# Kernel tuning notes

Measured on AMD Instinct MI355X. Metric: run time of the kernel, lower is better.

Reference implementation:

```python
import jax, jax.numpy as jnp
import numpy as np

N, CIN, H, W = 4, 64, 160, 256
INS_PER = 16
T = N * INS_PER            # total instances = sum(num_ins)
CH, OUT = 16, 1
WN = [(CIN + 2) * CH, CH * CH, CH * OUT]   # [1056, 256, 16]
BN = [CH, CH, OUT]
P = sum(WN) + sum(BN)      # 1361
MASK_BIAS_SHIFT = 2.19


def setup_inputs() -> dict:
    key = jax.random.key(0)
    k1, k2 = jax.random.split(key)
    x = jax.random.normal(k1, (N, CIN, H, W), dtype=jnp.float32)
    mask_head_params = jax.random.normal(k2, (T, P), dtype=jnp.float32) * 0.1
    num_ins = jnp.full((N,), INS_PER, dtype=jnp.int32)
    return {"x": x, "mask_head_params": mask_head_params, "num_ins": num_ins}


def reference(x, mask_head_params, num_ins):
    n, c, h, w = x.shape
    # compute_locations with stride=1: locations = stack((shift_x, shift_y)) + 0
    # NOTE: the original `locations[:0] /= H` / `locations[:1] /= W` are
    # zero-size slices (no-ops), so coords remain unnormalized.
    ys, xs = jnp.meshgrid(jnp.arange(h, dtype=jnp.float32),
                          jnp.arange(w, dtype=jnp.float32), indexing='ij')
    loc = jnp.stack([xs, ys], axis=0)                       # [2, H, W]
    loc = jnp.broadcast_to(loc[None], (n, 2, h, w))
    xc = jnp.concatenate([loc, x], axis=1)                  # [N, C+2, H, W]

    # per-image repeat -> one feature copy per instance
    feat = jnp.repeat(xc, num_ins, axis=0, total_repeat_length=T)  # [T, C+2, H, W]

    # parse dynamic params (mask=True: last bias shifted by -2.19)
    p = mask_head_params
    o = 0
    w0 = p[:, o:o + WN[0]].reshape(T, CH, CIN + 2); o += WN[0]
    w1 = p[:, o:o + WN[1]].reshape(T, CH, CH);      o += WN[1]
    w2 = p[:, o:o + WN[2]].reshape(T, OUT, CH);     o += WN[2]
    b0 = p[:, o:o + BN[0]]; o += BN[0]
    b1 = p[:, o:o + BN[1]]; o += BN[1]
    b2 = p[:, o:o + BN[2]] - MASK_BIAS_SHIFT

    # grouped 1x1 convs (groups=num_insts) == per-instance linear over HxW
    hdn = jax.nn.relu(jnp.einsum('toi,tihw->tohw', w0, feat) + b0[:, :, None, None])
    hdn = jax.nn.relu(jnp.einsum('toi,tihw->tohw', w1, hdn) + b1[:, :, None, None])
    out = jnp.einsum('toi,tihw->tohw', w2, hdn) + b2[:, :, None, None]
    return out.reshape(1, T * OUT, h, w)
```

## Files before the change

kernel.cpp:

```cpp
#include <hip/hip_runtime.h>


#define CIN  64
#define HH   160
#define WW   256
#define HWSZ (HH * WW)
#define PP   1361
#define MASK_BIAS_SHIFT 2.19f
#define PKF  2112
#define NSPLIT 2

typedef short short8 __attribute__((ext_vector_type(8)));
typedef float f32x4  __attribute__((ext_vector_type(4)));

union BF8 { short8 s; __bf16 b[8]; };


__global__ __launch_bounds__(64) void prep_params(
    const float* __restrict__ params, float* __restrict__ pk)
{
    const int t    = blockIdx.x;
    const int lane = threadIdx.x;
    const int col  = lane & 15;
    const int g    = lane >> 4;
    const float* pw = params + (size_t)t * PP;
    float* dst = pk + (size_t)t * PKF;

    BF8 a00, a01, a1;
#pragma unroll
    for (int j = 0; j < 8; ++j) {
        a00.b[j] = (__bf16)pw[col * 66 + 2 +      g * 8 + j];
        a01.b[j] = (__bf16)pw[col * 66 + 2 + 32 + g * 8 + j];
    }
#pragma unroll
    for (int j = 0; j < 4; ++j) {
        a1.b[j]     = (__bf16)pw[1056 + col * 16 + g * 4 + j];
        a1.b[4 + j] = (__bf16)0.f;
    }
    ((short8*)(dst      ))[lane] = a00.s;
    ((short8*)(dst + 256))[lane] = a01.s;
    ((short8*)(dst + 512))[lane] = a1.s;

    f32x4 wx, wy, b0, b1, w2;
#pragma unroll
    for (int j = 0; j < 4; ++j) {
        const int r = g * 4 + j;
        wx[j] = pw[r * 66 + 0];
        wy[j] = pw[r * 66 + 1];
        b0[j] = pw[1328 + r];
        b1[j] = pw[1344 + r];
        w2[j] = pw[1312 + r];
    }
    ((f32x4*)(dst +  768))[lane] = wx;
    ((f32x4*)(dst + 1024))[lane] = wy;
    ((f32x4*)(dst + 1280))[lane] = b0;
    ((f32x4*)(dst + 1536))[lane] = b1;
    ((f32x4*)(dst + 1792))[lane] = w2;
    if (lane == 0) dst[2048] = pw[1360] - MASK_BIAS_SHIFT;
}

__global__ __launch_bounds__(256, 4) void mask_head_mfma2(
    const float* __restrict__ x,
    const float* __restrict__ pk,
    const int*   __restrict__ num_ins,
    float*       __restrict__ out,
    int N, int T)
{
    const int tid  = threadIdx.x;
    const int wave = tid >> 6;
    const int lane = tid & 63;
    const int col  = lane & 15;
    const int g    = lane >> 4;
    const int n    = blockIdx.y;
    const int s    = blockIdx.z;
    const int pxw  = blockIdx.x * 256 + wave * 64;

    int t0 = 0;
    for (int j = 0; j < n; ++j) t0 += num_ins[j];
    int t1 = t0 + num_ins[n];
    if (n == N - 1) t1 = T;
    if (t1 > T) t1 = T;
    t0 = __builtin_amdgcn_readfirstlane(t0);
    t1 = __builtin_amdgcn_readfirstlane(t1);

    BF8 xb[4][2];
    const float* xbase = x + (size_t)n * CIN * HWSZ + pxw + col;
#pragma unroll
    for (int nt = 0; nt < 4; ++nt)
#pragma unroll
        for (int c = 0; c < 2; ++c)
#pragma unroll
            for (int j = 0; j < 8; ++j) {
                const int ch = c * 32 + g * 8 + j;
                xb[nt][c].b[j] = (__bf16)xbase[(size_t)ch * HWSZ + nt * 16];
            }

    float xf[4], yf[4];
#pragma unroll
    for (int nt = 0; nt < 4; ++nt) {
        const int pix = pxw + nt * 16 + col;
        xf[nt] = (float)(pix & (WW - 1));
        yf[nt] = (float)(pix >> 8);
    }

    for (int t = t0 + s; t < t1; t += NSPLIT) {
        const float* pt = pk + (size_t)t * PKF;

        short8 a00 = ((const short8*)(pt      ))[lane];
        short8 a01 = ((const short8*)(pt + 256))[lane];
        short8 a1  = ((const short8*)(pt + 512))[lane];
        f32x4  wxv = ((const f32x4*)(pt +  768))[lane];
        f32x4  wyv = ((const f32x4*)(pt + 1024))[lane];
        f32x4  b0v = ((const f32x4*)(pt + 1280))[lane];
        f32x4  b1v = ((const f32x4*)(pt + 1536))[lane];
        f32x4  w2v = ((const f32x4*)(pt + 1792))[lane];
        const float b2v = pt[2048];

        f32x4 acc0[4];
#pragma unroll
        for (int nt = 0; nt < 4; ++nt) {
            f32x4 a = {0.f, 0.f, 0.f, 0.f};
            a = __builtin_amdgcn_mfma_f32_16x16x32_bf16(a00, xb[nt][0].s, a, 0, 0, 0);
            a = __builtin_amdgcn_mfma_f32_16x16x32_bf16(a01, xb[nt][1].s, a, 0, 0, 0);
            acc0[nt] = a;
        }

        BF8 h0[4];
#pragma unroll
        for (int nt = 0; nt < 4; ++nt) {
#pragma unroll
            for (int j = 0; j < 4; ++j) {
                float v = acc0[nt][j] + b0v[j];
                v = fmaf(wxv[j], xf[nt], v);
                v = fmaf(wyv[j], yf[nt], v);
                v = fmaxf(v, 0.f);
                h0[nt].b[j]     = (__bf16)v;
                h0[nt].b[4 + j] = (__bf16)0.f;
            }
        }

        f32x4 acc1[4];
#pragma unroll
        for (int nt = 0; nt < 4; ++nt) {
            f32x4 a = {0.f, 0.f, 0.f, 0.f};
            acc1[nt] = __builtin_amdgcn_mfma_f32_16x16x32_bf16(a1, h0[nt].s, a, 0, 0, 0);
        }

        float oval = 0.f;
#pragma unroll
        for (int nt = 0; nt < 4; ++nt) {
            float sum = 0.f;
#pragma unroll
            for (int j = 0; j < 4; ++j) {
                const float h = fmaxf(acc1[nt][j] + b1v[j], 0.f);
                sum = fmaf(w2v[j], h, sum);
            }
            sum += __shfl_xor(sum, 16, 64);
            sum += __shfl_xor(sum, 32, 64);
            if (nt == g) oval = sum + b2v;
        }
        out[(size_t)t * HWSZ + pxw + lane] = oval;
    }
}

__global__ __launch_bounds__(256) void mask_head_mfma_nows(
    const float* __restrict__ x,
    const float* __restrict__ params,
    const int*   __restrict__ num_ins,
    float*       __restrict__ out,
    int N, int T)
{
    const int tid  = threadIdx.x;
    const int wave = tid >> 6;
    const int lane = tid & 63;
    const int col  = lane & 15;
    const int g    = lane >> 4;
    const int n    = blockIdx.y;
    const int pxw  = blockIdx.x * 256 + wave * 64;

    int t0 = 0;
    for (int j = 0; j < n; ++j) t0 += num_ins[j];
    int t1 = t0 + num_ins[n];
    if (n == N - 1) t1 = T;
    if (t1 > T) t1 = T;

    BF8 xb[4][2];
    const float* xbase = x + (size_t)n * CIN * HWSZ + pxw + col;
#pragma unroll
    for (int nt = 0; nt < 4; ++nt)
#pragma unroll
        for (int c = 0; c < 2; ++c)
#pragma unroll
            for (int j = 0; j < 8; ++j)
                xb[nt][c].b[j] = (__bf16)xbase[(size_t)(c * 32 + g * 8 + j) * HWSZ + nt * 16];

    float xf[4], yf[4];
#pragma unroll
    for (int nt = 0; nt < 4; ++nt) {
        const int pix = pxw + nt * 16 + col;
        xf[nt] = (float)(pix & (WW - 1));
        yf[nt] = (float)(pix >> 8);
    }

    for (int t = t0; t < t1; ++t) {
        const float* pw = params + (size_t)t * PP;
        BF8 a00, a01, a1;
#pragma unroll
        for (int j = 0; j < 8; ++j) {
            a00.b[j] = (__bf16)pw[col * 66 + 2 +      g * 8 + j];
            a01.b[j] = (__bf16)pw[col * 66 + 2 + 32 + g * 8 + j];
        }
#pragma unroll
        for (int j = 0; j < 4; ++j) {
            a1.b[j]     = (__bf16)pw[1056 + col * 16 + g * 4 + j];
            a1.b[4 + j] = (__bf16)0.f;
        }
        float wxv[4], wyv[4], b0v[4], b1v[4], w2v[4];
#pragma unroll
        for (int j = 0; j < 4; ++j) {
            const int r = g * 4 + j;
            wxv[j] = pw[r * 66 + 0];
            wyv[j] = pw[r * 66 + 1];
            b0v[j] = pw[1328 + r];
            b1v[j] = pw[1344 + r];
            w2v[j] = pw[1312 + r];
        }
        const float b2v = pw[1360] - MASK_BIAS_SHIFT;

        f32x4 acc0[4];
#pragma unroll
        for (int nt = 0; nt < 4; ++nt) {
            f32x4 a = {0.f, 0.f, 0.f, 0.f};
            a = __builtin_amdgcn_mfma_f32_16x16x32_bf16(a00.s, xb[nt][0].s, a, 0, 0, 0);
            a = __builtin_amdgcn_mfma_f32_16x16x32_bf16(a01.s, xb[nt][1].s, a, 0, 0, 0);
            acc0[nt] = a;
        }
        BF8 h0[4];
#pragma unroll
        for (int nt = 0; nt < 4; ++nt)
#pragma unroll
            for (int j = 0; j < 4; ++j) {
                float v = acc0[nt][j] + b0v[j];
                v = fmaf(wxv[j], xf[nt], v);
                v = fmaf(wyv[j], yf[nt], v);
                v = fmaxf(v, 0.f);
                h0[nt].b[j]     = (__bf16)v;
                h0[nt].b[4 + j] = (__bf16)0.f;
            }
        f32x4 acc1[4];
#pragma unroll
        for (int nt = 0; nt < 4; ++nt) {
            f32x4 a = {0.f, 0.f, 0.f, 0.f};
            acc1[nt] = __builtin_amdgcn_mfma_f32_16x16x32_bf16(a1.s, h0[nt].s, a, 0, 0, 0);
        }
        float oval = 0.f;
#pragma unroll
        for (int nt = 0; nt < 4; ++nt) {
            float sum = 0.f;
#pragma unroll
            for (int j = 0; j < 4; ++j) {
                const float h = fmaxf(acc1[nt][j] + b1v[j], 0.f);
                sum = fmaf(w2v[j], h, sum);
            }
            sum += __shfl_xor(sum, 16, 64);
            sum += __shfl_xor(sum, 32, 64);
            if (nt == g) oval = sum + b2v;
        }
        out[(size_t)t * HWSZ + pxw + lane] = oval;
    }
}

extern "C" void kernel_launch(void* const* d_in, const int* in_sizes, int n_in,
                              void* d_out, int out_size, void* d_ws, size_t ws_size,
                              hipStream_t stream) {
    const float* x      = (const float*)d_in[0];
    const float* params = (const float*)d_in[1];
    const int*   nins   = (const int*)d_in[2];
    float*       out    = (float*)d_out;

    const int N = in_sizes[2];
    const int T = in_sizes[1] / PP;
    const size_t ws_needed = (size_t)T * PKF * sizeof(float);

    if (ws_size >= ws_needed) {
        float* pk = (float*)d_ws;
        prep_params<<<T, dim3(64), 0, stream>>>(params, pk);
        dim3 grid(HWSZ / 256, N, NSPLIT);
        mask_head_mfma2<<<grid, dim3(256), 0, stream>>>(x, pk, nins, out, N, T);
    } else {
        dim3 grid(HWSZ / 256, N);
        mask_head_mfma_nows<<<grid, dim3(256), 0, stream>>>(x, params, nins, out, N, T);
    }
}
```

Measured before the change: 34.01 us.

## Stage block pixels in swizzled LDS and split instances across waves

Each block now converts its 256-pixel row of input features to bf16 once into XOR-swizzled shared memory. Each wave then handles a different subset of instances and covers all 256 pixels, instead of every wave covering its own 64 pixels for every instance. This aims to cut per-wave parameter loads and register pressure and to simplify the coordinate terms (y is constant per block). In exchange it adds 32KB of LDS per block, a block-wide barrier, and LDS reads inside the hot loop, and it may limit occupancy.

```diff
diff --git a/kernel.cpp b/kernel.cpp
--- a/kernel.cpp
+++ b/kernel.cpp
@@ -59,13 +59,15 @@
     if (lane == 0) dst[2048] = pw[1360] - MASK_BIAS_SHIFT;
 }
 
-__global__ __launch_bounds__(256, 4) void mask_head_mfma2(
+__global__ __launch_bounds__(256, 4) void mask_head_lds(
     const float* __restrict__ x,
     const float* __restrict__ pk,
     const int*   __restrict__ num_ins,
     float*       __restrict__ out,
     int N, int T)
 {
+    __shared__ __align__(16) char xs[256 * CIN * 2];
+
     const int tid  = threadIdx.x;
     const int wave = tid >> 6;
     const int lane = tid & 63;
@@ -73,37 +75,34 @@
     const int g    = lane >> 4;
     const int n    = blockIdx.y;
     const int s    = blockIdx.z;
-    const int pxw  = blockIdx.x * 256 + wave * 64;
+    const int blockpx = blockIdx.x * 256;
+
+    {
+        const float* xb = x + (size_t)n * CIN * HWSZ + blockpx + tid;
+        const int swz = (tid & 7) << 4;
+        char* dst = xs + tid * 128;
+        for (int c8 = 0; c8 < 8; ++c8) {
+            BF8 v;
+#pragma unroll
+            for (int j = 0; j < 8; ++j)
+                v.b[j] = (__bf16)xb[(size_t)(c8 * 8 + j) * HWSZ];
+            *(short8*)(dst + ((c8 * 16) ^ swz)) = v.s;
+        }
+    }
+    __syncthreads();
 
     int t0 = 0;
     for (int j = 0; j < n; ++j) t0 += num_ins[j];
     int t1 = t0 + num_ins[n];
     if (n == N - 1) t1 = T;
     if (t1 > T) t1 = T;
-    t0 = __builtin_amdgcn_readfirstlane(t0);
-    t1 = __builtin_amdgcn_readfirstlane(t1);
-
-    BF8 xb[4][2];
-    const float* xbase = x + (size_t)n * CIN * HWSZ + pxw + col;
-#pragma unroll
-    for (int nt = 0; nt < 4; ++nt)
-#pragma unroll
-        for (int c = 0; c < 2; ++c)
-#pragma unroll
-            for (int j = 0; j < 8; ++j) {
-                const int ch = c * 32 + g * 8 + j;
-                xb[nt][c].b[j] = (__bf16)xbase[(size_t)ch * HWSZ + nt * 16];
-            }
-
-    float xf[4], yf[4];
-#pragma unroll
-    for (int nt = 0; nt < 4; ++nt) {
-        const int pix = pxw + nt * 16 + col;
-        xf[nt] = (float)(pix & (WW - 1));
-        yf[nt] = (float)(pix >> 8);
-    }
-
-    for (int t = t0 + s; t < t1; t += NSPLIT) {
+    const int M = t1 - t0;
+
+    const float yf   = (float)blockIdx.x;
+    const float colf = (float)col;
+
+    for (int m = s + NSPLIT * wave; m < M; m += NSPLIT * 4) {
+        const int t = t0 + m;
         const float* pt = pk + (size_t)t * PKF;
 
         short8 a00 = ((const short8*)(pt      ))[lane];
@@ -116,50 +115,49 @@
         f32x4  w2v = ((const f32x4*)(pt + 1792))[lane];
         const float b2v = pt[2048];
 
-        f32x4 acc0[4];
-#pragma unroll
-        for (int nt = 0; nt < 4; ++nt) {
-            f32x4 a = {0.f, 0.f, 0.f, 0.f};
-            a = __builtin_amdgcn_mfma_f32_16x16x32_bf16(a00, xb[nt][0].s, a, 0, 0, 0);
-            a = __builtin_amdgcn_mfma_f32_16x16x32_bf16(a01, xb[nt][1].s, a, 0, 0, 0);
-            acc0[nt] = a;
-        }
-
-        BF8 h0[4];
-#pragma unroll
-        for (int nt = 0; nt < 4; ++nt) {
-#pragma unroll
-            for (int j = 0; j < 4; ++j) {
-                float v = acc0[nt][j] + b0v[j];
-                v = fmaf(wxv[j], xf[nt], v);
-                v = fmaf(wyv[j], yf[nt], v);
+        f32x4 bb;
+#pragma unroll
+        for (int j = 0; j < 4; ++j) bb[j] = fmaf(wyv[j], yf, b0v[j]);
+
+        float oval = 0.f;
+#pragma unroll
+        for (int nt = 0; nt < 16; ++nt) {
+            const int px   = nt * 16 + col;
+            const int rswz = (px & 7) << 4;
+            const char* src = xs + px * 128;
+            short8 xb0 = *(const short8*)(src + ((      g * 16) ^ rswz));
+            short8 xb1 = *(const short8*)(src + ((64 + g * 16) ^ rswz));
+
+            f32x4 acc0 = {0.f, 0.f, 0.f, 0.f};
+            acc0 = __builtin_amdgcn_mfma_f32_16x16x32_bf16(a00, xb0, acc0, 0, 0, 0);
+            acc0 = __builtin_amdgcn_mfma_f32_16x16x32_bf16(a01, xb1, acc0, 0, 0, 0);
+
+            const float xf = colf + (float)(nt * 16);
+            BF8 h0;
+#pragma unroll
+            for (int j = 0; j < 4; ++j) {
+                float v = acc0[j] + bb[j];
+                v = fmaf(wxv[j], xf, v);
                 v = fmaxf(v, 0.f);
-                h0[nt].b[j]     = (__bf16)v;
-                h0[nt].b[4 + j] = (__bf16)0.f;
-            }
-        }
-
-        f32x4 acc1[4];
-#pragma unroll
-        for (int nt = 0; nt < 4; ++nt) {
-            f32x4 a = {0.f, 0.f, 0.f, 0.f};
-            acc1[nt] = __builtin_amdgcn_mfma_f32_16x16x32_bf16(a1, h0[nt].s, a, 0, 0, 0);
-        }
-
-        float oval = 0.f;
-#pragma unroll
-        for (int nt = 0; nt < 4; ++nt) {
+                h0.b[j]     = (__bf16)v;
+                h0.b[4 + j] = (__bf16)0.f;
+            }
+
+            f32x4 acc1 = {0.f, 0.f, 0.f, 0.f};
+            acc1 = __builtin_amdgcn_mfma_f32_16x16x32_bf16(a1, h0.s, acc1, 0, 0, 0);
+
             float sum = 0.f;
 #pragma unroll
             for (int j = 0; j < 4; ++j) {
-                const float h = fmaxf(acc1[nt][j] + b1v[j], 0.f);
+                const float h = fmaxf(acc1[j] + b1v[j], 0.f);
                 sum = fmaf(w2v[j], h, sum);
             }
             sum += __shfl_xor(sum, 16, 64);
             sum += __shfl_xor(sum, 32, 64);
-            if (nt == g) oval = sum + b2v;
-        }
-        out[(size_t)t * HWSZ + pxw + lane] = oval;
+            if ((nt & 3) == g) oval = sum + b2v;
+            if ((nt & 3) == 3)
+                out[(size_t)t * HWSZ + blockpx + (nt >> 2) * 64 + lane] = oval;
+        }
     }
 }
 
@@ -285,8 +283,8 @@
     if (ws_size >= ws_needed) {
         float* pk = (float*)d_ws;
         prep_params<<<T, dim3(64), 0, stream>>>(params, pk);
-        dim3 grid(HWSZ / 256, N, NSPLIT);
-        mask_head_mfma2<<<grid, dim3(256), 0, stream>>>(x, pk, nins, out, N, T);
+        dim3 grid(HH, N, NSPLIT);
+        mask_head_lds<<<grid, dim3(256), 0, stream>>>(x, pk, nins, out, N, T);
     } else {
         dim3 grid(HWSZ / 256, N);
         mask_head_mfma_nows<<<grid, dim3(256), 0, stream>>>(x, params, nins, out, N, T);
```

After: 65.37 us. 1.92x slower.

## Fold biases, coordinate terms and final layer into MFMA instructions

Applied to the files above, without the earlier changes.

Moves the coordinate-channel weights and layer-0 bias into an extra MFMA, using a constant B-operand of pixel coords and ones with weights split into bf16 hi/lo parts. It also folds the layer-1 bias into the layer-1 MFMA through a ones row and replaces the shuffle-based final 16-to-1 reduction with a third MFMA. The packed parameter block shrinks and per-instance VALU work and cross-lane shuffles are removed, in exchange for two extra MFMAs per tile. The hidden layer is now rounded to bf16 before the last layer, and pixel coordinates up to 255 are stored in bf16, which cannot hold every integer above 256 exactly, so some accuracy may be lost.

```diff
diff --git a/kernel.cpp b/kernel.cpp
--- a/kernel.cpp
+++ b/kernel.cpp
@@ -7,13 +7,16 @@
 #define HWSZ (HH * WW)
 #define PP   1361
 #define MASK_BIAS_SHIFT 2.19f
-#define PKF  2112
+#define PKF  1344
 #define NSPLIT 2
 
 typedef short short8 __attribute__((ext_vector_type(8)));
 typedef float f32x4  __attribute__((ext_vector_type(4)));
 
 union BF8 { short8 s; __bf16 b[8]; };
+
+__device__ inline __bf16 bhi(float v) { return (__bf16)v; }
+__device__ inline __bf16 blo(float v) { return (__bf16)(v - (float)(__bf16)v); }
 
 
 __global__ __launch_bounds__(64) void prep_params(
@@ -26,40 +29,54 @@
     const float* pw = params + (size_t)t * PP;
     float* dst = pk + (size_t)t * PKF;
 
-    BF8 a00, a01, a1;
+    const __bf16 z = (__bf16)0.f;
+
+    BF8 a00, a01;
 #pragma unroll
     for (int j = 0; j < 8; ++j) {
         a00.b[j] = (__bf16)pw[col * 66 + 2 +      g * 8 + j];
         a01.b[j] = (__bf16)pw[col * 66 + 2 + 32 + g * 8 + j];
     }
-#pragma unroll
-    for (int j = 0; j < 4; ++j) {
-        a1.b[j]     = (__bf16)pw[1056 + col * 16 + g * 4 + j];
-        a1.b[4 + j] = (__bf16)0.f;
-    }
-    ((short8*)(dst      ))[lane] = a00.s;
-    ((short8*)(dst + 256))[lane] = a01.s;
-    ((short8*)(dst + 512))[lane] = a1.s;
-
-    f32x4 wx, wy, b0, b1, w2;
-#pragma unroll
-    for (int j = 0; j < 4; ++j) {
-        const int r = g * 4 + j;
-        wx[j] = pw[r * 66 + 0];
-        wy[j] = pw[r * 66 + 1];
-        b0[j] = pw[1328 + r];
-        b1[j] = pw[1344 + r];
-        w2[j] = pw[1312 + r];
-    }
-    ((f32x4*)(dst +  768))[lane] = wx;
-    ((f32x4*)(dst + 1024))[lane] = wy;
-    ((f32x4*)(dst + 1280))[lane] = b0;
-    ((f32x4*)(dst + 1536))[lane] = b1;
-    ((f32x4*)(dst + 1792))[lane] = w2;
-    if (lane == 0) dst[2048] = pw[1360] - MASK_BIAS_SHIFT;
-}
-
-__global__ __launch_bounds__(256, 4) void mask_head_mfma2(
+
+    BF8 a1b;
+#pragma unroll
+    for (int j = 0; j < 4; ++j)
+        a1b.b[j] = (__bf16)pw[1056 + col * 16 + g * 4 + j];
+    {
+        const float b1 = pw[1344 + col];
+        a1b.b[4] = (g == 0) ? bhi(b1) : z;
+        a1b.b[5] = (g == 0) ? blo(b1) : z;
+        a1b.b[6] = z;  a1b.b[7] = z;
+    }
+
+    BF8 a2r;
+#pragma unroll
+    for (int j = 0; j < 4; ++j) a2r.b[j] = (__bf16)pw[1312 + g * 4 + j];
+    a2r.b[4] = z; a2r.b[5] = z; a2r.b[6] = z; a2r.b[7] = z;
+
+    BF8 ca;
+    {
+        const float wx = pw[col * 66 + 0];
+        const float wy = pw[col * 66 + 1];
+        const float b0 = pw[1328 + col];
+        ca.b[0] = (g == 0) ? bhi(wx) : z;
+        ca.b[1] = (g == 0) ? blo(wx) : z;
+        ca.b[2] = (g == 0) ? bhi(wy) : z;
+        ca.b[3] = (g == 0) ? blo(wy) : z;
+        ca.b[4] = (g == 0) ? bhi(b0) : z;
+        ca.b[5] = (g == 0) ? blo(b0) : z;
+        ca.b[6] = z; ca.b[7] = z;
+    }
+
+    ((short8*)(dst       ))[lane] = a00.s;
+    ((short8*)(dst +  256))[lane] = a01.s;
+    ((short8*)(dst +  512))[lane] = a1b.s;
+    ((short8*)(dst +  768))[lane] = a2r.s;
+    ((short8*)(dst + 1024))[lane] = ca.s;
+    if (lane == 0) dst[1280] = pw[1360] - MASK_BIAS_SHIFT;
+}
+
+__global__ __launch_bounds__(256, 4) void mask_head_v5(
     const float* __restrict__ x,
     const float* __restrict__ pk,
     const int*   __restrict__ num_ins,
@@ -95,69 +112,55 @@
                 xb[nt][c].b[j] = (__bf16)xbase[(size_t)ch * HWSZ + nt * 16];
             }
 
-    float xf[4], yf[4];
+    BF8 b2c[4];
 #pragma unroll
     for (int nt = 0; nt < 4; ++nt) {
-        const int pix = pxw + nt * 16 + col;
-        xf[nt] = (float)(pix & (WW - 1));
-        yf[nt] = (float)(pix >> 8);
-    }
+        const int px = pxw + nt * 16 + col;
+        const __bf16 xfb = (__bf16)(float)(px & (WW - 1));
+        const __bf16 yfb = (__bf16)(float)(px >> 8);
+        b2c[nt].b[0] = xfb; b2c[nt].b[1] = xfb;
+        b2c[nt].b[2] = yfb; b2c[nt].b[3] = yfb;
+        b2c[nt].b[4] = (__bf16)1.f; b2c[nt].b[5] = (__bf16)1.f;
+        b2c[nt].b[6] = (__bf16)0.f; b2c[nt].b[7] = (__bf16)0.f;
+    }
+
+    const __bf16 one = (__bf16)1.f, zero = (__bf16)0.f;
 
     for (int t = t0 + s; t < t1; t += NSPLIT) {
         const float* pt = pk + (size_t)t * PKF;
 
-        short8 a00 = ((const short8*)(pt      ))[lane];
-        short8 a01 = ((const short8*)(pt + 256))[lane];
-        short8 a1  = ((const short8*)(pt + 512))[lane];
-        f32x4  wxv = ((const f32x4*)(pt +  768))[lane];
-        f32x4  wyv = ((const f32x4*)(pt + 1024))[lane];
-        f32x4  b0v = ((const f32x4*)(pt + 1280))[lane];
-        f32x4  b1v = ((const f32x4*)(pt + 1536))[lane];
-        f32x4  w2v = ((const f32x4*)(pt + 1792))[lane];
-        const float b2v = pt[2048];
-
-        f32x4 acc0[4];
-#pragma unroll
-        for (int nt = 0; nt < 4; ++nt) {
-            f32x4 a = {0.f, 0.f, 0.f, 0.f};
-            a = __builtin_amdgcn_mfma_f32_16x16x32_bf16(a00, xb[nt][0].s, a, 0, 0, 0);
-            a = __builtin_amdgcn_mfma_f32_16x16x32_bf16(a01, xb[nt][1].s, a, 0, 0, 0);
-            acc0[nt] = a;
-        }
-
-        BF8 h0[4];
-#pragma unroll
-        for (int nt = 0; nt < 4; ++nt) {
-#pragma unroll
-            for (int j = 0; j < 4; ++j) {
-                float v = acc0[nt][j] + b0v[j];
-                v = fmaf(wxv[j], xf[nt], v);
-                v = fmaf(wyv[j], yf[nt], v);
-                v = fmaxf(v, 0.f);
-                h0[nt].b[j]     = (__bf16)v;
-                h0[nt].b[4 + j] = (__bf16)0.f;
-            }
-        }
-
-        f32x4 acc1[4];
-#pragma unroll
-        for (int nt = 0; nt < 4; ++nt) {
-            f32x4 a = {0.f, 0.f, 0.f, 0.f};
-            acc1[nt] = __builtin_amdgcn_mfma_f32_16x16x32_bf16(a1, h0[nt].s, a, 0, 0, 0);
-        }
+        short8 a00 = ((const short8*)(pt       ))[lane];
+        short8 a01 = ((const short8*)(pt +  256))[lane];
+        short8 a1b = ((const short8*)(pt +  512))[lane];
+        short8 a2r = ((const short8*)(pt +  768))[lane];
+        short8 ca  = ((const short8*)(pt + 1024))[lane];
+        const float b2v = pt[1280];
 
         float oval = 0.f;
 #pragma unroll
         for (int nt = 0; nt < 4; ++nt) {
-            float sum = 0.f;
-#pragma unroll
-            for (int j = 0; j < 4; ++j) {
-                const float h = fmaxf(acc1[nt][j] + b1v[j], 0.f);
-                sum = fmaf(w2v[j], h, sum);
-            }
-            sum += __shfl_xor(sum, 16, 64);
-            sum += __shfl_xor(sum, 32, 64);
-            if (nt == g) oval = sum + b2v;
+            f32x4 acc0 = {0.f, 0.f, 0.f, 0.f};
+            acc0 = __builtin_amdgcn_mfma_f32_16x16x32_bf16(ca,  b2c[nt].s,  acc0, 0, 0, 0);
+            acc0 = __builtin_amdgcn_mfma_f32_16x16x32_bf16(a00, xb[nt][0].s, acc0, 0, 0, 0);
+            acc0 = __builtin_amdgcn_mfma_f32_16x16x32_bf16(a01, xb[nt][1].s, acc0, 0, 0, 0);
+
+            BF8 h0;
+#pragma unroll
+            for (int j = 0; j < 4; ++j) h0.b[j] = (__bf16)fmaxf(acc0[j], 0.f);
+            h0.b[4] = one; h0.b[5] = one; h0.b[6] = zero; h0.b[7] = zero;
+
+            f32x4 acc1 = {0.f, 0.f, 0.f, 0.f};
+            acc1 = __builtin_amdgcn_mfma_f32_16x16x32_bf16(a1b, h0.s, acc1, 0, 0, 0);
+
+            BF8 h1;
+#pragma unroll
+            for (int j = 0; j < 4; ++j) h1.b[j] = (__bf16)fmaxf(acc1[j], 0.f);
+            h1.b[4] = zero; h1.b[5] = zero; h1.b[6] = zero; h1.b[7] = zero;
+
+            f32x4 acc2 = {0.f, 0.f, 0.f, 0.f};
+            acc2 = __builtin_amdgcn_mfma_f32_16x16x32_bf16(a2r, h1.s, acc2, 0, 0, 0);
+
+            if (nt == g) oval = acc2[0] + b2v;
         }
         out[(size_t)t * HWSZ + pxw + lane] = oval;
     }
@@ -286,7 +289,7 @@
         float* pk = (float*)d_ws;
         prep_params<<<T, dim3(64), 0, stream>>>(params, pk);
         dim3 grid(HWSZ / 256, N, NSPLIT);
-        mask_head_mfma2<<<grid, dim3(256), 0, stream>>>(x, pk, nins, out, N, T);
+        mask_head_v5<<<grid, dim3(256), 0, stream>>>(x, pk, nins, out, N, T);
     } else {
         dim3 grid(HWSZ / 256, N);
         mask_head_mfma_nows<<<grid, dim3(256), 0, stream>>>(x, params, nins, out, N, T);
```

New measurement: 31.17 us. -8.4%, faster.
